# Optimization experiments

Measured on AMD Instinct MI355X. Metric: run time of the kernel, lower is better.

Reference implementation:

```python
import jax, jax.numpy as jnp
import numpy as np
from jax import lax

H_IMG, W_IMG = 1280, 1280
STRIDES = (8, 16, 32, 64, 128)
FEAT_SHAPES = tuple((H_IMG // s) * (W_IMG // s) for s in STRIDES)  # (25600,6400,1600,400,100)
N_POINTS = sum(FEAT_SHAPES)  # 34100
NUM_CLASSES = 1
TOPK = 1000
SCORE_THRESH = 0.05
NMS_THRESH = 0.5
MAX_DET = 300
BATCH = 8
N_GT = 200


def make_points():
    # matches AnchorFreePS.reference_points: cell centers at stride*i + stride//2, (cx, cy) order
    pts = []
    for s in STRIDES:
        h, w = H_IMG // s, W_IMG // s
        cx = np.arange(w, dtype=np.float32) * s + s // 2
        cy = np.arange(h, dtype=np.float32) * s + s // 2
        gy, gx = np.meshgrid(cy, cx, indexing='ij')
        pts.append(np.stack([gx, gy], axis=-1).reshape(-1, 2))
    return jnp.asarray(np.concatenate(pts, axis=0))


def setup_inputs() -> dict:
    key = jax.random.key(0)
    k1, k2, k3, k4 = jax.random.split(key, 4)
    points = make_points()  # [N,2]
    xy = jax.random.uniform(k1, (BATCH, N_GT, 2), minval=0.0, maxval=1000.0)
    wh = jax.random.uniform(k2, (BATCH, N_GT, 2), minval=20.0, maxval=260.0)
    gt_boxes = jnp.concatenate([xy, xy + wh], axis=-1)  # [B,M,4] x1y1x2y2
    cls_logits = jax.random.normal(k3, (BATCH, N_POINTS, NUM_CLASSES)) * 1.5 - 3.0
    regression = jax.random.uniform(k4, (BATCH, N_POINTS, 4)) * 0.1  # normalized ltrb codes
    return {"points": points, "gt_boxes": gt_boxes, "cls_logits": cls_logits, "regression": regression}


def match_points_to_boxes(points, gt_boxes):
    # point-in-box test + area-cost argmin (compute_loss matched_idxs)
    px = points[None, :, None, 0]  # [1,N,1]
    py = points[None, :, None, 1]
    b = gt_boxes[:, None, :, :]    # [B,1,M,4]
    inside = (px >= b[..., 0]) & (px <= b[..., 2]) & (py >= b[..., 1]) & (py <= b[..., 3])  # [B,N,M]
    matched = jnp.any(inside, axis=-1)  # [B,N]
    areas = (gt_boxes[..., 2] - gt_boxes[..., 0]) * (gt_boxes[..., 3] - gt_boxes[..., 1])  # [B,M]
    BIG = jnp.float32(2 ** 31 - 1)  # torch.iinfo(torch.int).max
    cost = jnp.where(inside, areas[:, None, :], BIG)
    idx = jnp.argmin(cost, axis=-1)
    return jnp.where(matched, idx, -1)


def decode_boxes(rel, pts):
    # FCOSBoxCoder.decode_single with weights (1,1,1,1)
    l = rel[:, 0] * W_IMG
    t = rel[:, 1] * H_IMG
    r = rel[:, 2] * W_IMG
    b = rel[:, 3] * H_IMG
    x, y = pts[:, 0], pts[:, 1]
    return jnp.stack([x - l, y - t, x + r, y + b], axis=-1)


def clip_boxes(boxes):
    return jnp.stack([
        jnp.clip(boxes[:, 0], 0.0, W_IMG),
        jnp.clip(boxes[:, 1], 0.0, H_IMG),
        jnp.clip(boxes[:, 2], 0.0, W_IMG),
        jnp.clip(boxes[:, 3], 0.0, H_IMG)], axis=-1)


def nms(boxes, scores, labels, valid_init):
    # fixed-size sequential NMS equivalent to batched_nms (same-label suppression)
    work = lax.stop_gradient(jnp.where(valid_init, scores, -jnp.inf))

    def body(w, _):
        i = jnp.argmax(w)
        s = w[i]
        box = boxes[i]
        x1 = jnp.maximum(box[0], boxes[:, 0])
        y1 = jnp.maximum(box[1], boxes[:, 1])
        x2 = jnp.minimum(box[2], boxes[:, 2])
        y2 = jnp.minimum(box[3], boxes[:, 3])
        inter = jnp.clip(x2 - x1, 0.0) * jnp.clip(y2 - y1, 0.0)
        a1 = (box[2] - box[0]) * (box[3] - box[1])
        a2 = (boxes[:, 2] - boxes[:, 0]) * (boxes[:, 3] - boxes[:, 1])
        iou = inter / (a1 + a2 - inter + 1e-9)
        supp = (iou > NMS_THRESH) & (labels == labels[i])
        w = jnp.where(supp, -jnp.inf, w).at[i].set(-jnp.inf)
        return w, (i, s)

    _, (idxs, picked) = lax.scan(body, work, None, length=MAX_DET)
    valid = picked > -jnp.inf
    return idxs, valid


def postprocess_image(points, cls_i, reg_i):
    bx_list, sc_list, lb_list = [], [], []
    off = 0
    for size in FEAT_SHAPES:  # fixed small level loop
        sl = slice(off, off + size)
        off += size
        scores = jax.nn.sigmoid(cls_i[sl]).reshape(-1)  # [size*C]
        k = min(TOPK, size * NUM_CLASSES)
        sc, idx = lax.top_k(scores, k)
        a = idx // NUM_CLASSES
        lb = idx % NUM_CLASSES
        bx = clip_boxes(decode_boxes(reg_i[sl][a], points[sl][a]))
        bx_list.append(bx)
        sc_list.append(sc)
        lb_list.append(lb)
    boxes = jnp.concatenate(bx_list, axis=0)
    scores = jnp.concatenate(sc_list, axis=0)
    labels = jnp.concatenate(lb_list, axis=0)
    idxs, valid = nms(boxes, scores, labels, scores > SCORE_THRESH)
    out_boxes = jnp.where(valid[:, None], boxes[idxs], 0.0)
    out_scores = jnp.where(valid, scores[idxs], 0.0)
    out_labels = jnp.where(valid, labels[idxs], -1)
    return out_boxes, out_scores, out_labels, valid


def reference(points, gt_boxes, cls_logits, regression):
    matched_idxs = match_points_to_boxes(points, gt_boxes)  # [B,N]
    boxes, scores, labels, valid = jax.vmap(
        lambda c, r: postprocess_image(points, c, r))(cls_logits, regression)
    return matched_idxs, boxes, scores, labels, valid
```

## Files before the change

### kernel.cpp

```cpp
#include <hip/hip_runtime.h>
#include <stdint.h>

#define N_POINTS   34100
#define BATCH      8
#define N_GT       200
#define NLEV       5
#define NCAND      3500
#define MAX_DET    300
#define SCORE_TH   0.05f
#define NMS_TH     0.5f
#define IMG        1280.0f
#define NBIN       4096
#define TIE_CAP    4096
#define MTH 0.50000002980232238769531250

#define OUT_MATCH  0
#define OUT_BOXES  272800
#define OUT_SCORES 282400
#define OUT_LABELS 284800
#define OUT_VALID  287200

#define WS_KEYS    0
#define WS_SBOX    2632192
#define WS_SSC     3080192
#define WS_MASK    3192192
#define WS_DIAG    9500032
#define WS_HIST    WS_MASK
#define HSUB       8
#define MASK_STRIDE 98560
#define DIAG_STRIDE 3520


typedef unsigned long long u64;
typedef uint32_t u32;

__device__ __forceinline__ int mask_off(int c) {
    int g = c >> 6;
    return 64 * (55 * g - (g * (g - 1)) / 2) + (c - (g << 6)) * (55 - g);
}

__device__ __forceinline__ int level_of(int p) {
    return (p < 25600) ? 0 : (p < 32000) ? 1 : (p < 33600) ? 2 : (p < 34000) ? 3 : 4;
}
__device__ __forceinline__ int loff_of(int l) {
    return (l == 0) ? 0 : (l == 1) ? 25600 : (l == 2) ? 32000 : (l == 3) ? 33600 : 34000;
}
__device__ __forceinline__ int k_of(int l) {
    return (l == 0) ? 1000 : (l == 1) ? 1000 : (l == 2) ? 1000 : (l == 3) ? 400 : 100;
}
__device__ __forceinline__ u64 readlane64(u64 v, int t) {
    u32 lo = (u32)__builtin_amdgcn_readlane((int)(u32)v, t);
    u32 hi = (u32)__builtin_amdgcn_readlane((int)(u32)(v >> 32), t);
    return ((u64)hi << 32) | lo;
}

__global__ __launch_bounds__(1024)
void match_hist_kernel(const float* __restrict__ points,
                       const float* __restrict__ gt,
                       const float* __restrict__ logits,
                       float* __restrict__ out_match,
                       u32* __restrict__ keys,
                       u32* __restrict__ ghist) {
#pragma clang fp contract(off)
    __shared__ float bx1[N_GT], by1[N_GT], bx2[N_GT], by2[N_GT], ar[N_GT];
    __shared__ u32 hh[NBIN];
    const int b = blockIdx.x & 7;
    const int g = blockIdx.x >> 3;
    const int tid = threadIdx.x;

    if (g < 17) {
        const int base = g * 2048 + tid;
        for (int j = tid; j < N_GT; j += 1024) {
            float x1 = gt[(b * N_GT + j) * 4 + 0];
            float y1 = gt[(b * N_GT + j) * 4 + 1];
            float x2 = gt[(b * N_GT + j) * 4 + 2];
            float y2 = gt[(b * N_GT + j) * 4 + 3];
            bx1[j] = x1; by1[j] = y1; bx2[j] = x2; by2[j] = y2;
            ar[j] = (x2 - x1) * (y2 - y1);
        }
        __syncthreads();

        const float BIGF = 2147483648.0f;
        float px[2], py[2], best[2];
        int bi[2];
#pragma unroll
        for (int k = 0; k < 2; ++k) {
            int p = base + k * 1024;
            int pc = (p < N_POINTS) ? p : 0;
            px[k] = points[pc * 2 + 0];
            py[k] = points[pc * 2 + 1];
            best[k] = BIGF; bi[k] = -1;
        }
        for (int j = 0; j < N_GT; ++j) {
            float x1 = bx1[j], y1 = by1[j], x2 = bx2[j], y2 = by2[j], a = ar[j];
#pragma unroll
            for (int k = 0; k < 2; ++k) {
                bool inside = (px[k] >= x1) && (px[k] <= x2) &&
                              (py[k] >= y1) && (py[k] <= y2);
                float cost = inside ? a : BIGF;
                if (cost < best[k]) { best[k] = cost; bi[k] = j; }
            }
        }
#pragma unroll
        for (int k = 0; k < 2; ++k) {
            int p = base + k * 1024;
            if (p >= N_POINTS) continue;
            out_match[b * N_POINTS + p] = (float)bi[k];
        }
    } else {
        const int f = g - 17;
        int lev, sub, p0, cnt;
        if (f < 8)       { lev = 0; sub = f;     p0 = f * 3200;               cnt = 3200; }
        else if (f < 10) { lev = 1; sub = f - 8; p0 = 25600 + (f - 8) * 3200; cnt = 3200; }
        else if (f == 10){ lev = 2; sub = 0;     p0 = 32000;                  cnt = 1600; }
        else if (f == 11){ lev = 3; sub = 0;     p0 = 33600;                  cnt = 400;  }
        else             { lev = 4; sub = 0;     p0 = 34000;                  cnt = 100;  }

        for (int i = tid; i < NBIN; i += 1024) hh[i] = 0u;
        __syncthreads();

        for (int i = tid; i < cnt; i += 1024) {
            int p = p0 + i;
            float lg = logits[b * N_POINTS + p];
            float s = 1.0f / (1.0f + expf(-lg));
            u32 u = __float_as_uint(s);
            u32 key = (u & 0x80000000u) ? ~u : (u | 0x80000000u);
            keys[b * N_POINTS + p] = key;
            atomicAdd(&hh[(key >> 19) & 4095u], 1u);
        }
        __syncthreads();

        u32* outp = ghist + (((u32)b * NLEV + (u32)lev) * HSUB + (u32)sub) * NBIN;
        for (int i = tid; i < NBIN; i += 1024) outp[i] = hh[i];
    }
}

#define SEL_OFF(b) ((((u32)(b) * NLEV + 4) * HSUB + 7) * NBIN)

#define LSWZ(j) (((j) & 63) * 65 + ((j) >> 6))
__global__ __launch_bounds__(1024)
void select_kernel(u32* __restrict__ ghist) {
    __shared__ u32 lsb[5 * 4160];
    __shared__ u32 sTl[NLEV], skkl[NLEV];
    const int b = blockIdx.x;
    const int tid = threadIdx.x;
    const int lane = tid & 63;
    const int wid = tid >> 6;

    {
        const u32* hb = ghist + (u32)b * (NLEV * HSUB * NBIN);
#pragma unroll
        for (int lev = 0; lev < NLEV; ++lev) {
            const int SUBS = (lev == 0) ? 8 : (lev == 1) ? 2 : 1;
            const u32* hl = hb + lev * HSUB * NBIN + tid;
            u32 s0 = 0, s1 = 0, s2 = 0, s3 = 0;
#pragma unroll
            for (int sub = 0; sub < SUBS; ++sub) {
                const u32* hs = hl + sub * NBIN;
                s0 += hs[0]; s1 += hs[1024]; s2 += hs[2048]; s3 += hs[3072];
            }
            u32* lv = lsb + lev * 4160;
            lv[LSWZ(tid)]        = s0;
            lv[LSWZ(tid + 1024)] = s1;
            lv[LSWZ(tid + 2048)] = s2;
            lv[LSWZ(tid + 3072)] = s3;
        }
    }
    __syncthreads();

    if (wid < NLEV) {
        const u32 K = (u32)k_of(wid);
        const u32* hh = lsb + wid * 4160;
        u32 S = 0;
#pragma unroll 16
        for (int i = 0; i < 64; ++i) S += hh[i * 65 + lane];
        u32 acc = S;
#pragma unroll
        for (int off = 1; off < 64; off <<= 1) {
            u32 v = (u32)__shfl_down((int)acc, off);
            if (lane + off < 64) acc += v;
        }
        u32 sfxAfter = acc - S;
        bool hit = (sfxAfter < K) && (sfxAfter + S >= K);
        u64 bal = __ballot(hit);
        int Lg = (int)__builtin_ctzll(bal);
        u32 sfxG = (u32)__shfl((int)sfxAfter, Lg);

        u32 v = hh[lane * 65 + Lg];
        u32 acc2 = v;
#pragma unroll
        for (int off = 1; off < 64; off <<= 1) {
            u32 t = (u32)__shfl_down((int)acc2, off);
            if (lane + off < 64) acc2 += t;
        }
        u32 sfx2 = sfxG + acc2 - v;
        bool hit2 = (sfx2 < K) && (sfx2 + v >= K);
        if (hit2) { sTl[wid] = (u32)(Lg * 64 + lane); skkl[wid] = K - sfx2; }
    }
    __syncthreads();
    if (tid < NLEV) {
        u32* selp = ghist + SEL_OFF(b);
        selp[tid] = sTl[tid];
        selp[NLEV + tid] = skkl[tid];
    }
}

#define SORT_T 1024
__global__ __launch_bounds__(SORT_T)
void compact_kernel(const u32* __restrict__ keys,
                    const u32* __restrict__ ghist,
                    const float* __restrict__ reg,
                    const float* __restrict__ points,
                    float* __restrict__ sboxes,
                    float* __restrict__ sscores) {
#pragma clang fp contract(off)
    __shared__ __align__(16) char smem[131072];
    u64* sk   = (u64*)smem;
    u64* tb   = (u64*)(smem + 32768);
    u64* aux  = (u64*)(smem + 65536);
    u32* h    = (u32*)(smem + 98304);
    u32* bs   = (u32*)(smem + 114688);
    __shared__ u32 sTl[NLEV], skkl[NLEV], wt[16];
    __shared__ u32 scnt, stcnt;

    const int b = blockIdx.x;
    const int tid = threadIdx.x;
    const int lane = tid & 63;
    const int wid = tid >> 6;
    const u32* kk_ = keys + b * N_POINTS;

    if (tid == 0) { scnt = 0u; stcnt = 0u; }
    if (tid < NLEV) {
        const u32* selp = ghist + SEL_OFF(b);
        sTl[tid] = selp[tid];
        skkl[tid] = selp[NLEV + tid];
    }

    {
        const uint4* kp4 = (const uint4*)kk_;
        u32 a0 = 0, a1 = 0, a2 = 0, a3 = 0;
        int i = tid;
        for (; i + 3072 < 8525; i += 4096) {
            uint4 v0 = kp4[i];
            uint4 v1 = kp4[i + 1024];
            uint4 v2 = kp4[i + 2048];
            uint4 v3 = kp4[i + 3072];
            a0 ^= v0.x ^ v0.y ^ v0.z ^ v0.w;
            a1 ^= v1.x ^ v1.y ^ v1.z ^ v1.w;
            a2 ^= v2.x ^ v2.y ^ v2.z ^ v2.w;
            a3 ^= v3.x ^ v3.y ^ v3.z ^ v3.w;
        }
        for (; i < 8525; i += 1024) {
            uint4 v = kp4[i];
            a0 ^= v.x ^ v.y ^ v.z ^ v.w;
        }
        u32 wacc = a0 ^ a1 ^ a2 ^ a3;
        asm volatile("" :: "v"(wacc));
    }
    __syncthreads();

    const u64 below = (lane == 0) ? 0ull : (~0ull >> (64 - lane));
    const int CHUNK = 4 * SORT_T;
    for (int it = 0; it < (N_POINTS + CHUNK - 1) / CHUNK; ++it) {
        u32 key4[4]; int pc4[4]; bool act4[4];
#pragma unroll
        for (int u = 0; u < 4; ++u) {
            int i = it * CHUNK + u * SORT_T + tid;
            act4[u] = (i < N_POINTS);
            pc4[u] = act4[u] ? i : (N_POINTS - 1);
            key4[u] = kk_[pc4[u]];
        }
#pragma unroll
        for (int u = 0; u < 4; ++u) {
            bool active = act4[u];
            int pc = pc4[u];
            u32 key = key4[u];
            int l = level_of(pc);
            u32 digit = (key >> 19) & 4095u;
            u32 T = sTl[l];
            bool isDef = active && (digit > T);
            bool isTie = active && (digit == T);
            u64 k50 = ((u64)key << 18) | ((u64)(7 - l) << 15)
                    | (u64)(32767 - (pc - loff_of(l)));
            u64 grp = __ballot(isDef);
            if (grp) {
                int leader = (int)__builtin_ctzll(grp);
                u32 base_ = 0;
                if (lane == leader)
                    base_ = atomicAdd(&scnt, (u32)__builtin_popcountll(grp));
                base_ = (u32)__shfl((int)base_, leader);
                if (isDef) sk[base_ + (u32)__builtin_popcountll(grp & below)] = k50;
            }
            u64 tg = __ballot(isTie);
            if (tg) {
                int leader = (int)__builtin_ctzll(tg);
                u32 base_ = 0;
                if (lane == leader)
                    base_ = atomicAdd(&stcnt, (u32)__builtin_popcountll(tg));
                base_ = (u32)__shfl((int)base_, leader);
                if (isTie) {
                    u32 pos = base_ + (u32)__builtin_popcountll(tg & below);
                    if (pos < TIE_CAP) tb[pos] = k50;
                }
            }
        }
    }
    __syncthreads();

    int t = (int)stcnt; if (t > TIE_CAP) t = TIE_CAP;
    for (int j0 = tid; j0 - tid < t; j0 += SORT_T) {
        bool active = j0 < t;
        u64 kj = active ? tb[j0] : 0ull;
        u32 lvtag = (u32)(kj >> 15) & 7u;
        int r = 0;
        for (int i = 0; i < t; ++i) {
            u64 ki = tb[i];
            r += (ki > kj && (((u32)(ki >> 15) & 7u) == lvtag)) ? 1 : 0;
        }
        bool inc = active && (r < (int)skkl[7 - lvtag]);
        u64 grp = __ballot(inc);
        if (grp) {
            int leader = (int)__builtin_ctzll(grp);
            u32 base_ = 0;
            if (lane == leader)
                base_ = atomicAdd(&scnt, (u32)__builtin_popcountll(grp));
            base_ = (u32)__shfl((int)base_, leader);
            if (inc) sk[base_ + (u32)__builtin_popcountll(grp & below)] = kj;
        }
    }
    __syncthreads();
    const int total = (int)scnt;

    for (int i = tid; i < NBIN; i += SORT_T) h[i] = 0u;
    __syncthreads();
    for (int i = tid; i < total; i += SORT_T)
        atomicAdd(&h[(u32)(sk[i] >> 37) & 4095u], 1u);
    __syncthreads();

    u32 t0 = h[4095 - 4 * tid];
    u32 t1 = h[4095 - (4 * tid + 1)];
    u32 t2 = h[4095 - (4 * tid + 2)];
    u32 t3 = h[4095 - (4 * tid + 3)];
    u32 tsum = t0 + t1 + t2 + t3;
    u32 sc_ = tsum;
#pragma unroll
    for (int off = 1; off < 64; off <<= 1) {
        u32 v = (u32)__shfl_up((int)sc_, off);
        if (lane >= off) sc_ += v;
    }
    if (lane == 63) wt[wid] = sc_;
    __syncthreads();
    if (tid < 64) {
        u32 v = (tid < 16) ? wt[tid] : 0u;
        u32 s2 = v;
#pragma unroll
        for (int off = 1; off < 16; off <<= 1) {
            u32 x = (u32)__shfl_up((int)s2, off);
            if (tid >= off) s2 += x;
        }
        if (tid < 16) wt[tid] = s2 - v;
    }
    __syncthreads();
    u32 run = (sc_ - tsum) + wt[wid];
    bs[4095 - 4 * tid] = run;       run += t0;
    bs[4095 - (4 * tid + 1)] = run; run += t1;
    bs[4095 - (4 * tid + 2)] = run; run += t2;
    bs[4095 - (4 * tid + 3)] = run;
    __syncthreads();
    for (int i = tid; i < NBIN; i += SORT_T) h[i] = 0u;
    __syncthreads();
    for (int i = tid; i < total; i += SORT_T) {
        u64 k = sk[i];
        u32 d = (u32)(k >> 37) & 4095u;
        u32 pos = bs[d] + atomicAdd(&h[d], 1u);
        aux[pos] = k;
    }
    __syncthreads();
    for (int p = tid; p < total; p += SORT_T) {
        u64 kp = aux[p];
        u32 d = (u32)(kp >> 37) & 4095u;
        u32 gbase = bs[d];
        u32 gend = (d == 0) ? (u32)total : bs[d - 1];
        u32 r = 0;
        for (u32 q = gbase; q < gend; ++q) r += (aux[q] > kp) ? 1u : 0u;
        sk[gbase + r] = kp;
    }
    __syncthreads();

    for (int r = tid; r < NCAND; r += SORT_T) {
        float x1 = 0.f, y1 = 0.f, x2 = 0.f, y2 = 0.f, sc = 0.f;
        if (r < total) {
            u64 k50 = sk[r];
            int lowb = (int)(k50 & 0x3FFFFull);
            int l = 7 - (lowb >> 15);
            int idxl = 32767 - (lowb & 32767);
            int p = loff_of(l) + idxl;
            u32 key32 = (u32)(k50 >> 18);
            sc = __uint_as_float(key32 ^ 0x80000000u);
            int gp = b * N_POINTS + p;
            float l_ = reg[gp * 4 + 0] * IMG;
            float t_ = reg[gp * 4 + 1] * IMG;
            float r_ = reg[gp * 4 + 2] * IMG;
            float bb = reg[gp * 4 + 3] * IMG;
            float px = points[p * 2 + 0];
            float py = points[p * 2 + 1];
            x1 = fminf(fmaxf(px - l_, 0.0f), IMG);
            y1 = fminf(fmaxf(py - t_, 0.0f), IMG);
            x2 = fminf(fmaxf(px + r_, 0.0f), IMG);
            y2 = fminf(fmaxf(py + bb, 0.0f), IMG);
        }
        int slot = b * NCAND + r;
        sboxes[slot * 4 + 0] = x1;
        sboxes[slot * 4 + 1] = y1;
        sboxes[slot * 4 + 2] = x2;
        sboxes[slot * 4 + 3] = y2;
        sscores[slot] = sc;
    }
}

__global__ __launch_bounds__(256)
void mask_kernel(const float* __restrict__ sboxes,
                 const float* __restrict__ sscores,
                 u64* __restrict__ mask,
                 u64* __restrict__ diag) {
#pragma clang fp contract(off)
    const int b = blockIdx.x & 7;
    const int gx = blockIdx.x >> 3;
    const int wv = threadIdx.x >> 6;
    const int lane = threadIdx.x & 63;
    const int NG = (NCAND + 3) >> 2;
    const int NH = (NG + 1) >> 1;
    const int gidx = gx * 4 + wv;
    if (gidx >= NH) return;

    const float4* gb = (const float4*)sboxes + b * NCAND;
    const float* gs = sscores + b * NCAND;
    u64* mout = mask + (size_t)b * MASK_STRIDE;
    u64* dout = diag + (size_t)b * DIAG_STRIDE;

    for (int s = 0; s < 2; ++s) {
        const int g0 = (s == 0) ? gidx : (NG - 1 - gidx);
        if (s == 1 && g0 == gidx) break;
        const int c0 = g0 << 2;

        float4 bc[4]; float a1[4]; bool ok[4]; int g[4]; u64* rp[4];
        bool any = false;
#pragma unroll
        for (int i = 0; i < 4; ++i) {
            int c = c0 + i;
            int cc = (c < NCAND) ? c : (NCAND - 1);
            bc[i] = gb[cc];
            a1[i] = (bc[i].z - bc[i].x) * (bc[i].w - bc[i].y);
            ok[i] = (c < NCAND) && (gs[cc] > SCORE_TH);
            g[i] = cc >> 6;
            rp[i] = mout + mask_off(cc) - g[i];
            any |= ok[i];
        }
        if (!any) continue;

        for (int w = (c0 >> 6); w < 55; ++w) {
            int cj = (w << 6) + lane;
            float4 bj = (cj < NCAND) ? gb[cj] : make_float4(0.f, 0.f, 0.f, 0.f);
            float a2 = (bj.z - bj.x) * (bj.w - bj.y);
#pragma unroll
            for (int i = 0; i < 4; ++i) {
                float x1 = fmaxf(bc[i].x, bj.x);
                float y1 = fmaxf(bc[i].y, bj.y);
                float x2 = fminf(bc[i].z, bj.z);
                float y2 = fminf(bc[i].w, bj.w);
                float inter = fmaxf(x2 - x1, 0.f) * fmaxf(y2 - y1, 0.f);
                float denom = a1[i] + a2 - inter + 1e-9f;
                float hf = 0.5f * denom;
                float rr = fmaf(0x1p-25f, denom, hf);
                u64 bits = __ballot(inter > rr);
                u64 eq = __ballot(inter == rr);
                if (eq) {
                    u64 fb = __ballot((double)inter > MTH * (double)denom);
                    bits |= (eq & fb);
                }
                if (lane == 0 && ok[i] && w >= g[i]) {
                    rp[i][w] = bits;
                    if (w == g[i]) dout[c0 + i] = bits;
                }
            }
        }
    }
}

__global__ __launch_bounds__(1024)
void scan_kernel(const float* __restrict__ sboxes,
                 const float* __restrict__ sscores,
                 const u64* __restrict__ mask,
                 const u64* __restrict__ diag,
                 float* __restrict__ out) {
    __shared__ u32 pick_idx[MAX_DET];
    const int b = blockIdx.x;
    const int tid = threadIdx.x;
    const u64* mrow = mask + (size_t)b * MASK_STRIDE;
    const u64* drow = diag + (size_t)b * DIAG_STRIDE;
    const float4* gb = (const float4*)sboxes + b * NCAND;
    const float* gs = sscores + b * NCAND;

    if (tid >= 64) {
        const uint4* mp = (const uint4*)mrow;
        const uint4* dp = (const uint4*)drow;
        const uint4* bp = (const uint4*)gb;
        const uint4* sp = (const uint4*)gs;
        const int t = tid - 64;
        u32 a0 = 0, a1 = 0, a2 = 0, a3 = 0, a4 = 0, a5 = 0, a6 = 0, a7 = 0;
        int i = t;
        for (; i + 6720 < 49280; i += 7680) {
            uint4 v0 = mp[i];
            uint4 v1 = mp[i + 960];
            uint4 v2 = mp[i + 1920];
            uint4 v3 = mp[i + 2880];
            uint4 v4 = mp[i + 3840];
            uint4 v5 = mp[i + 4800];
            uint4 v6 = mp[i + 5760];
            uint4 v7 = mp[i + 6720];
            a0 ^= v0.x ^ v0.y ^ v0.z ^ v0.w;
            a1 ^= v1.x ^ v1.y ^ v1.z ^ v1.w;
            a2 ^= v2.x ^ v2.y ^ v2.z ^ v2.w;
            a3 ^= v3.x ^ v3.y ^ v3.z ^ v3.w;
            a4 ^= v4.x ^ v4.y ^ v4.z ^ v4.w;
            a5 ^= v5.x ^ v5.y ^ v5.z ^ v5.w;
            a6 ^= v6.x ^ v6.y ^ v6.z ^ v6.w;
            a7 ^= v7.x ^ v7.y ^ v7.z ^ v7.w;
        }
        for (; i < 49280; i += 960) {
            uint4 v = mp[i];
            a0 ^= v.x ^ v.y ^ v.z ^ v.w;
        }
        if (t < 880) {
            uint4 v0 = dp[t];
            uint4 v1 = dp[t + 880];
            a1 ^= v0.x ^ v0.y ^ v0.z ^ v0.w;
            a2 ^= v1.x ^ v1.y ^ v1.z ^ v1.w;
        }
        for (int j = t; j < 3500; j += 960) {
            uint4 v = bp[j];
            a3 ^= v.x ^ v.y ^ v.z ^ v.w;
        }
        if (t < 875) {
            uint4 v = sp[t];
            a4 ^= v.x ^ v.y ^ v.z ^ v.w;
        }
        u32 acc = (a0 ^ a1) ^ (a2 ^ a3) ^ (a4 ^ a5) ^ (a6 ^ a7);
        asm volatile("" :: "v"(acc));
        return;
    }

    const int lane = tid;

    float* ob = out + OUT_BOXES  + b * MAX_DET * 4;
    float* os = out + OUT_SCORES + b * MAX_DET;
    float* ol = out + OUT_LABELS + b * MAX_DET;
    float* ov = out + OUT_VALID  + b * MAX_DET;

    u64 m = 0ull;
    u64 rowN = drow[lane];
    float sjN = gs[lane];

    int kept = 0;
    for (int w = 0; w < 55; ++w) {
        const int wbase = w << 6;
        const u64 row = rowN;
        const float sj = sjN;
        if (w < 54) {
            int cn = wbase + 64 + lane;
            int cc = (cn < NCAND) ? cn : (NCAND - 1);
            rowN = drow[cc];
            float s = gs[cc];
            sjN = (cn < NCAND) ? s : 0.f;
        }
        int c = wbase + lane;
        u64 bad = __ballot(!((c < NCAND) && (sj > SCORE_TH)));
        u64 cur = readlane64(m, w) | bad;
        u64 km = 0ull;
        while (kept < MAX_DET) {
            u64 avail = ~cur;
            if (avail == 0ull) break;
            int t = (int)__builtin_ctzll(avail);
            u64 r = readlane64(row, t);
            cur |= r | (1ull << t);
            km |= 1ull << t;
            if (lane == 0) pick_idx[kept] = (u32)(wbase + t);
            kept++;
        }
        if (km) {
            const bool lr = (lane >= w && lane < 55);
            const int lo = lane - w;
            u64 acc = 0ull;
            while (km) {
#define POPBIT(tn) int tn = -1; if (km) { tn = (int)__builtin_ctzll(km); km &= km - 1ull; }
                POPBIT(t0) POPBIT(t1) POPBIT(t2) POPBIT(t3)
                POPBIT(t4) POPBIT(t5) POPBIT(t6) POPBIT(t7)
#undef POPBIT
                u64 v0 = 0, v1 = 0, v2 = 0, v3 = 0, v4 = 0, v5 = 0, v6 = 0, v7 = 0;
                if (lr) {
                    v0 = mrow[mask_off(wbase + t0) + lo];
                    if (t1 >= 0) v1 = mrow[mask_off(wbase + t1) + lo];
                    if (t2 >= 0) v2 = mrow[mask_off(wbase + t2) + lo];
                    if (t3 >= 0) v3 = mrow[mask_off(wbase + t3) + lo];
                    if (t4 >= 0) v4 = mrow[mask_off(wbase + t4) + lo];
                    if (t5 >= 0) v5 = mrow[mask_off(wbase + t5) + lo];
                    if (t6 >= 0) v6 = mrow[mask_off(wbase + t6) + lo];
                    if (t7 >= 0) v7 = mrow[mask_off(wbase + t7) + lo];
                }
                acc |= ((v0 | v1) | (v2 | v3)) | ((v4 | v5) | (v6 | v7));
            }
            m |= acc;
        }
        if (kept >= MAX_DET) break;
    }

    for (int k = lane; k < kept; k += 64) {
        u32 c = pick_idx[k];
        float4 bx = gb[c];
        float s = gs[c];
        ob[k * 4 + 0] = bx.x;
        ob[k * 4 + 1] = bx.y;
        ob[k * 4 + 2] = bx.z;
        ob[k * 4 + 3] = bx.w;
        os[k] = s;
        ol[k] = 0.0f;
        ov[k] = 1.0f;
    }
    for (int k = kept + lane; k < MAX_DET; k += 64) {
        ob[k * 4 + 0] = 0.f; ob[k * 4 + 1] = 0.f;
        ob[k * 4 + 2] = 0.f; ob[k * 4 + 3] = 0.f;
        os[k] = 0.f; ol[k] = -1.f; ov[k] = 0.f;
    }
}

extern "C" void kernel_launch(void* const* d_in, const int* in_sizes, int n_in,
                              void* d_out, int out_size, void* d_ws, size_t ws_size,
                              hipStream_t stream) {
    const float* points = (const float*)d_in[0];
    const float* gt     = (const float*)d_in[1];
    const float* logits = (const float*)d_in[2];
    const float* reg    = (const float*)d_in[3];
    float* out = (float*)d_out;

    u32* keys      = (u32*)((char*)d_ws + WS_KEYS);
    float* sboxes  = (float*)((char*)d_ws + WS_SBOX);
    float* sscores = (float*)((char*)d_ws + WS_SSC);
    u64* mask   = (u64*)((char*)d_ws + WS_MASK);
    u64* diag   = (u64*)((char*)d_ws + WS_DIAG);
    u32* ghist  = (u32*)((char*)d_ws + WS_HIST);

    match_hist_kernel<<<30 * BATCH, 1024, 0, stream>>>(points, gt, logits,
                                                       out + OUT_MATCH, keys, ghist);

    select_kernel<<<BATCH, 1024, 0, stream>>>(ghist);

    compact_kernel<<<BATCH, SORT_T, 0, stream>>>(keys, ghist, reg, points,
                                                 sboxes, sscores);

    mask_kernel<<<110 * BATCH, 256, 0, stream>>>(sboxes, sscores, mask, diag);

    scan_kernel<<<BATCH, 1024, 0, stream>>>(sboxes, sscores, mask, diag, out);
}
```

Measured before the change: 230.0 us.

## Split candidate compaction across 64 blocks with global atomics, separate sort kernel

The compaction pass that scanned all 34100 keys per image in a single block now runs in 8 slices per image (64 blocks). Each slice appends to global candidate and tie buffers through global atomic counters, and a new sort kernel loads those buffers into shared memory and continues the original tie-resolution and sort. This spreads the serial per-image scan over more CUs. It costs an extra kernel launch, a memset, global atomic traffic, and a round trip through global memory. Candidate order in the buffer becomes nondeterministic, which the later sort must absorb. The tie buffer capacity also shrinks to 2048.

```diff
diff --git a/kernel.cpp b/kernel.cpp
--- a/kernel.cpp
+++ b/kernel.cpp
@@ -11,7 +11,6 @@
 #define NMS_TH     0.5f
 #define IMG        1280.0f
 #define NBIN       4096
-#define TIE_CAP    4096
 #define MTH 0.50000002980232238769531250
 
 #define OUT_MATCH  0
@@ -21,6 +20,11 @@
 #define OUT_VALID  287200
 
 #define WS_KEYS    0
+#define WS_CAND    1091200
+#define WS_TIEB    1353344
+#define WS_CNT     1484416
+#define CAND_CAP   4096
+#define TIEB_CAP   2048
 #define WS_SBOX    2632192
 #define WS_SSC     3080192
 #define WS_MASK    3192192
@@ -205,68 +209,37 @@
     }
 }
 
-#define SORT_T 1024
-__global__ __launch_bounds__(SORT_T)
+#define SLICE_PTS 4263
+__global__ __launch_bounds__(1024)
 void compact_kernel(const u32* __restrict__ keys,
                     const u32* __restrict__ ghist,
-                    const float* __restrict__ reg,
-                    const float* __restrict__ points,
-                    float* __restrict__ sboxes,
-                    float* __restrict__ sscores) {
-#pragma clang fp contract(off)
-    __shared__ __align__(16) char smem[131072];
-    u64* sk   = (u64*)smem;
-    u64* tb   = (u64*)(smem + 32768);
-    u64* aux  = (u64*)(smem + 65536);
-    u32* h    = (u32*)(smem + 98304);
-    u32* bs   = (u32*)(smem + 114688);
-    __shared__ u32 sTl[NLEV], skkl[NLEV], wt[16];
-    __shared__ u32 scnt, stcnt;
-
-    const int b = blockIdx.x;
+                    u64* __restrict__ cand,
+                    u64* __restrict__ tieb,
+                    u32* __restrict__ cnts) {
+    __shared__ u32 sTl[NLEV];
+    const int b = blockIdx.x & 7;
+    const int sl = blockIdx.x >> 3;
     const int tid = threadIdx.x;
     const int lane = tid & 63;
-    const int wid = tid >> 6;
+    if (tid < NLEV) sTl[tid] = ghist[SEL_OFF(b) + tid];
+    __syncthreads();
+
     const u32* kk_ = keys + b * N_POINTS;
-
-    if (tid == 0) { scnt = 0u; stcnt = 0u; }
-    if (tid < NLEV) {
-        const u32* selp = ghist + SEL_OFF(b);
-        sTl[tid] = selp[tid];
-        skkl[tid] = selp[NLEV + tid];
-    }
-
-    {
-        const uint4* kp4 = (const uint4*)kk_;
-        u32 a0 = 0, a1 = 0, a2 = 0, a3 = 0;
-        int i = tid;
-        for (; i + 3072 < 8525; i += 4096) {
-            uint4 v0 = kp4[i];
-            uint4 v1 = kp4[i + 1024];
-            uint4 v2 = kp4[i + 2048];
-            uint4 v3 = kp4[i + 3072];
-            a0 ^= v0.x ^ v0.y ^ v0.z ^ v0.w;
-            a1 ^= v1.x ^ v1.y ^ v1.z ^ v1.w;
-            a2 ^= v2.x ^ v2.y ^ v2.z ^ v2.w;
-            a3 ^= v3.x ^ v3.y ^ v3.z ^ v3.w;
-        }
-        for (; i < 8525; i += 1024) {
-            uint4 v = kp4[i];
-            a0 ^= v.x ^ v.y ^ v.z ^ v.w;
-        }
-        u32 wacc = a0 ^ a1 ^ a2 ^ a3;
-        asm volatile("" :: "v"(wacc));
-    }
-    __syncthreads();
-
+    u64* cb = cand + b * CAND_CAP;
+    u64* tbg = tieb + b * TIEB_CAP;
+    u32* cnt = cnts + b;
+    u32* tcnt = cnts + 8 + b;
+    const int p0 = sl * SLICE_PTS;
+    const int p1 = (p0 + SLICE_PTS < N_POINTS) ? (p0 + SLICE_PTS) : N_POINTS;
     const u64 below = (lane == 0) ? 0ull : (~0ull >> (64 - lane));
-    const int CHUNK = 4 * SORT_T;
-    for (int it = 0; it < (N_POINTS + CHUNK - 1) / CHUNK; ++it) {
+
+    const int CH = 4 * 1024;
+    for (int it = p0; it < p1; it += CH) {
         u32 key4[4]; int pc4[4]; bool act4[4];
 #pragma unroll
         for (int u = 0; u < 4; ++u) {
-            int i = it * CHUNK + u * SORT_T + tid;
-            act4[u] = (i < N_POINTS);
+            int i = it + u * 1024 + tid;
+            act4[u] = (i < p1);
             pc4[u] = act4[u] ? i : (N_POINTS - 1);
             key4[u] = kk_[pc4[u]];
         }
@@ -287,27 +260,62 @@
                 int leader = (int)__builtin_ctzll(grp);
                 u32 base_ = 0;
                 if (lane == leader)
-                    base_ = atomicAdd(&scnt, (u32)__builtin_popcountll(grp));
+                    base_ = atomicAdd(cnt, (u32)__builtin_popcountll(grp));
                 base_ = (u32)__shfl((int)base_, leader);
-                if (isDef) sk[base_ + (u32)__builtin_popcountll(grp & below)] = k50;
+                if (isDef) cb[base_ + (u32)__builtin_popcountll(grp & below)] = k50;
             }
             u64 tg = __ballot(isTie);
             if (tg) {
                 int leader = (int)__builtin_ctzll(tg);
                 u32 base_ = 0;
                 if (lane == leader)
-                    base_ = atomicAdd(&stcnt, (u32)__builtin_popcountll(tg));
+                    base_ = atomicAdd(tcnt, (u32)__builtin_popcountll(tg));
                 base_ = (u32)__shfl((int)base_, leader);
                 if (isTie) {
                     u32 pos = base_ + (u32)__builtin_popcountll(tg & below);
-                    if (pos < TIE_CAP) tb[pos] = k50;
+                    if (pos < TIEB_CAP) tbg[pos] = k50;
                 }
             }
         }
     }
-    __syncthreads();
-
-    int t = (int)stcnt; if (t > TIE_CAP) t = TIE_CAP;
+}
+
+#define SORT_T 1024
+__global__ __launch_bounds__(SORT_T)
+void sort_kernel(const u64* __restrict__ cand,
+                 const u64* __restrict__ tieb,
+                 const u32* __restrict__ cnts,
+                 const u32* __restrict__ ghist,
+                 const float* __restrict__ reg,
+                 const float* __restrict__ points,
+                 float* __restrict__ sboxes,
+                 float* __restrict__ sscores) {
+#pragma clang fp contract(off)
+    __shared__ __align__(16) char smem[131072];
+    u64* sk   = (u64*)smem;
+    u64* tb   = (u64*)(smem + 32768);
+    u64* aux  = (u64*)(smem + 65536);
+    u32* h    = (u32*)(smem + 98304);
+    u32* bs   = (u32*)(smem + 114688);
+    __shared__ u32 skkl[NLEV], wt[16];
+    __shared__ u32 scnt;
+
+    const int b = blockIdx.x;
+    const int tid = threadIdx.x;
+    const int lane = tid & 63;
+    const int wid = tid >> 6;
+
+    const int n = (int)cnts[b];
+    int t = (int)cnts[8 + b];
+    if (t > TIEB_CAP) t = TIEB_CAP;
+    if (tid == 0) scnt = (u32)n;
+    if (tid < NLEV) skkl[tid] = ghist[SEL_OFF(b) + NLEV + tid];
+
+    for (int i = tid; i < n; i += SORT_T) sk[i] = cand[b * CAND_CAP + i];
+    for (int i = tid; i < t; i += SORT_T) tb[i] = tieb[b * TIEB_CAP + i];
+    __syncthreads();
+
+    const u64 below = (lane == 0) ? 0ull : (~0ull >> (64 - lane));
     for (int j0 = tid; j0 - tid < t; j0 += SORT_T) {
         bool active = j0 < t;
         u64 kj = active ? tb[j0] : 0ull;
@@ -643,19 +651,26 @@
     float* out = (float*)d_out;
 
     u32* keys      = (u32*)((char*)d_ws + WS_KEYS);
+    u64* cand      = (u64*)((char*)d_ws + WS_CAND);
+    u64* tieb      = (u64*)((char*)d_ws + WS_TIEB);
+    u32* cnts      = (u32*)((char*)d_ws + WS_CNT);
     float* sboxes  = (float*)((char*)d_ws + WS_SBOX);
     float* sscores = (float*)((char*)d_ws + WS_SSC);
     u64* mask   = (u64*)((char*)d_ws + WS_MASK);
     u64* diag   = (u64*)((char*)d_ws + WS_DIAG);
     u32* ghist  = (u32*)((char*)d_ws + WS_HIST);
 
+    hipMemsetAsync(cnts, 0, 16 * sizeof(u32), stream);
+
     match_hist_kernel<<<30 * BATCH, 1024, 0, stream>>>(points, gt, logits,
                                                        out + OUT_MATCH, keys, ghist);
 
     select_kernel<<<BATCH, 1024, 0, stream>>>(ghist);
 
-    compact_kernel<<<BATCH, SORT_T, 0, stream>>>(keys, ghist, reg, points,
-                                                 sboxes, sscores);
+    compact_kernel<<<8 * BATCH, 1024, 0, stream>>>(keys, ghist, cand, tieb, cnts);
+
+    sort_kernel<<<BATCH, SORT_T, 0, stream>>>(cand, tieb, cnts, ghist, reg, points,
+                                              sboxes, sscores);
 
     mask_kernel<<<110 * BATCH, 256, 0, stream>>>(sboxes, sscores, mask, diag);
 
```

New measurement: 283.2 us. +23.1%, slower.
